# Kernel tuning notes

Hardware: AMD Instinct MI355X
Metric: run time of the kernel (lower is better)

## Reference

```python
import jax, jax.numpy as jnp
import numpy as np

B, S, D_IN, D_H, D_OUT = 8, 4096, 512, 1024, 512


def setup_inputs() -> dict:
    key = jax.random.key(0)
    ks = jax.random.split(key, 7)
    # scale weights by 1/sqrt(fan_in) so activations stay O(1) through the ReLU stack
    return {
        "query": jax.random.normal(ks[0], (B, S, D_IN), dtype=jnp.float32),
        "W0": jax.random.normal(ks[1], (B, D_H, D_IN), dtype=jnp.float32) * (D_IN ** -0.5),
        "b0": jax.random.normal(ks[2], (B, D_H), dtype=jnp.float32) * 0.02,
        "W1": jax.random.normal(ks[3], (B, D_H, D_H), dtype=jnp.float32) * (D_H ** -0.5),
        "b1": jax.random.normal(ks[4], (B, D_H), dtype=jnp.float32) * 0.02,
        "W2": jax.random.normal(ks[5], (B, D_OUT, D_H), dtype=jnp.float32) * (D_H ** -0.5),
        "b2": jax.random.normal(ks[6], (B, D_OUT), dtype=jnp.float32) * 0.02,
    }


def reference(query, W0, b0, W1, b1, W2, b2):
    # Original loops over (seq, batch) issuing F.linear per sample with per-batch
    # weights; this is exactly a batched GEMM over the batch axis.
    # F.linear(x, w, b) = x @ w.T + b, with w[b] of shape [out, in].
    h = jax.nn.relu(jnp.einsum('bsd,bhd->bsh', query, W0) + b0[:, None, :])  # [B,S,H]
    h = jax.nn.relu(jnp.einsum('bsh,bgh->bsg', h, W1) + b1[:, None, :])      # [B,S,H]
    out = jnp.einsum('bsg,bog->bso', h, W2) + b2[:, None, :]                 # [B,S,O]
    return out
```

## Files before the change

### kernel.cpp

```cpp
#include <hip/hip_runtime.h>


typedef _Float16 f16x8 __attribute__((ext_vector_type(8)));
typedef _Float16 f16x4 __attribute__((ext_vector_type(4)));
typedef float    f32x4 __attribute__((ext_vector_type(4)));

__device__ __forceinline__ void stage16(const void* g, void* l) {
    __builtin_amdgcn_global_load_lds(
        (const __attribute__((address_space(1))) unsigned int*)g,
        (__attribute__((address_space(3))) unsigned int*)l,
        16, 0, 0);
}

template <int CNT> __device__ __forceinline__ void vmwait() {
    if constexpr (CNT == 8)      asm volatile("s_waitcnt vmcnt(8)");
    else if constexpr (CNT == 4) asm volatile("s_waitcnt vmcnt(4)");
    else                         asm volatile("s_waitcnt vmcnt(0)");
}
__device__ __forceinline__ void barrier_() {
    __builtin_amdgcn_sched_barrier(0);
    __builtin_amdgcn_s_barrier();
}

__device__ __forceinline__ void cast_seg(const float* __restrict__ s,
                                         _Float16* __restrict__ d, int n4) {
    const int stride = gridDim.x * 256;
    for (int i = blockIdx.x * 256 + threadIdx.x; i < n4; i += stride) {
        float4 f = reinterpret_cast<const float4*>(s)[i];
        f16x4 o;
        o[0] = (_Float16)f.x; o[1] = (_Float16)f.y;
        o[2] = (_Float16)f.z; o[3] = (_Float16)f.w;
        reinterpret_cast<f16x4*>(d)[i] = o;
    }
}

__global__ __launch_bounds__(256) void cast_all(
    const float* s0, _Float16* d0, int n0,
    const float* s1, _Float16* d1, int n1,
    const float* s2, _Float16* d2, int n2,
    const float* s3, _Float16* d3, int n3) {
    cast_seg(s0, d0, n0);
    cast_seg(s1, d1, n1);
    cast_seg(s2, d2, n2);
    cast_seg(s3, d3, n3);
}

template <bool RELU, bool OUT_F16>
__global__ __launch_bounds__(512, 2) void gemm_olap(
    const _Float16* __restrict__ A, const _Float16* __restrict__ W,
    const float* __restrict__ bias, void* __restrict__ Outv,
    int M, int N, int K) {
    constexpr int BM = 256, BN = 256, BK = 32;
    constexpr int DEPTH = 4;
    __shared__ __align__(16) _Float16 As[DEPTH][BM * BK];
    __shared__ __align__(16) _Float16 Bs[DEPTH][BN * BK];

    const int tid  = threadIdx.x;
    const int lane = tid & 63;
    const int rowl = lane & 15;
    const int qswz = (((lane >> 4) ^ ((rowl >> 1) & 3)) * 8);
    const int w    = tid >> 6;
    const int wm   = (w >> 2) * 128;
    const int wn   = (w & 3) * 64;

    const int nwg = gridDim.x;
    const int cpx = nwg >> 3;
    const int sw  = (blockIdx.x & 7) * cpx + (blockIdx.x >> 3);
    const int MB  = M >> 8;
    const int NB  = N >> 8;
    const int bm  = sw % MB;
    const int rr  = sw / MB;
    const int bn  = rr % NB;
    const int b   = rr / NB;

    const int c0 = tid, c1 = tid + 512;
    const int ar0 = c0 >> 2, ar1 = c1 >> 2;
    const int ak0 = (((c0 & 3) ^ ((ar0 >> 1) & 3)) * 8);
    const int ak1 = (((c1 & 3) ^ ((ar1 >> 1) & 3)) * 8);

    const char* Ab = (const char*)(A + (size_t)b * M * K + (size_t)(bm * BM) * K);
    const char* Wb = (const char*)(W + (size_t)b * N * K + (size_t)(bn * BN) * K);
    size_t aoff0 = ((size_t)ar0 * K + ak0) * 2;
    size_t aoff1 = ((size_t)ar1 * K + ak1) * 2;
    size_t woff0 = ((size_t)ar0 * K + ak0) * 2;
    size_t woff1 = ((size_t)ar1 * K + ak1) * 2;
    constexpr size_t KSTEP = (size_t)BK * 2;

    f32x4 acc[8][4];
#pragma unroll
    for (int mi = 0; mi < 8; ++mi)
#pragma unroll
        for (int ni = 0; ni < 4; ++ni)
            acc[mi][ni] = (f32x4){0.f, 0.f, 0.f, 0.f};

    const int nk = K / BK;

#pragma unroll
    for (int p = 0; p < DEPTH - 1; ++p) {
        stage16(Ab + aoff0, &As[p][8 * (size_t)c0]);
        stage16(Ab + aoff1, &As[p][8 * (size_t)c1]);
        stage16(Wb + woff0, &Bs[p][8 * (size_t)c0]);
        stage16(Wb + woff1, &Bs[p][8 * (size_t)c1]);
        aoff0 += KSTEP; aoff1 += KSTEP; woff0 += KSTEP; woff1 += KSTEP;
    }
    vmwait<8>();
    barrier_();

    f16x8 afA[8], bfA[4], afB[8], bfB[4];

#define READS(AF, BF, SS)                                                     \
    BF[0] = *(const f16x8*)(&Bs[SS][(wn +  0 + rowl) * BK + qswz]);           \
    BF[1] = *(const f16x8*)(&Bs[SS][(wn + 16 + rowl) * BK + qswz]);           \
    BF[2] = *(const f16x8*)(&Bs[SS][(wn + 32 + rowl) * BK + qswz]);           \
    BF[3] = *(const f16x8*)(&Bs[SS][(wn + 48 + rowl) * BK + qswz]);           \
    _Pragma("unroll")                                                         \
    for (int mi = 0; mi < 8; ++mi)                                            \
        AF[mi] = *(const f16x8*)(&As[SS][(wm + mi * 16 + rowl) * BK + qswz]);

#define STAGE(SS)                                                             \
    stage16(Ab + aoff0, &As[SS][8 * (size_t)c0]);                             \
    stage16(Ab + aoff1, &As[SS][8 * (size_t)c1]);                             \
    stage16(Wb + woff0, &Bs[SS][8 * (size_t)c0]);                             \
    stage16(Wb + woff1, &Bs[SS][8 * (size_t)c1]);                             \
    aoff0 += KSTEP; aoff1 += KSTEP; woff0 += KSTEP; woff1 += KSTEP;

#define MFMA32(AF, BF)                                                        \
    __builtin_amdgcn_s_setprio(1);                                            \
    _Pragma("unroll")                                                         \
    for (int mi = 0; mi < 8; ++mi) {                                          \
        acc[mi][0] = __builtin_amdgcn_mfma_f32_16x16x32_f16(AF[mi], BF[0], acc[mi][0], 0, 0, 0); \
        acc[mi][1] = __builtin_amdgcn_mfma_f32_16x16x32_f16(AF[mi], BF[1], acc[mi][1], 0, 0, 0); \
        acc[mi][2] = __builtin_amdgcn_mfma_f32_16x16x32_f16(AF[mi], BF[2], acc[mi][2], 0, 0, 0); \
        acc[mi][3] = __builtin_amdgcn_mfma_f32_16x16x32_f16(AF[mi], BF[3], acc[mi][3], 0, 0, 0); \
    }                                                                         \
    __builtin_amdgcn_s_setprio(0);

    READS(afA, bfA, 0);

    for (int i = 0; i < nk / 2; ++i) {
        const int t0 = 2 * i, t1 = t0 + 1;

        if (t0 + 2 < nk) vmwait<4>(); else vmwait<0>();
        barrier_();
        if (t0 + 3 < nk) { STAGE((t0 + 3) & 3); }
        READS(afB, bfB, t1 & 3);
        MFMA32(afA, bfA);

        if (t1 + 2 < nk) vmwait<4>(); else vmwait<0>();
        barrier_();
        if (t1 + 3 < nk) { STAGE((t1 + 3) & 3); }
        if (t1 + 1 < nk) { READS(afA, bfA, (t1 + 1) & 3); }
        MFMA32(afB, bfB);
    }
#undef READS
#undef STAGE
#undef MFMA32

    const int q = lane >> 4;
    float bcol[4];
    {
        const float* bp = bias + (size_t)b * N + bn * BN + wn;
#pragma unroll
        for (int ni = 0; ni < 4; ++ni) bcol[ni] = bp[ni * 16 + rowl];
    }
#pragma unroll
    for (int mi = 0; mi < 8; ++mi) {
        const int row0 = bm * BM + wm + mi * 16 + q * 4;
#pragma unroll
        for (int r = 0; r < 4; ++r) {
            const size_t ro = (size_t)b * M * N + (size_t)(row0 + r) * N + bn * BN + wn;
#pragma unroll
            for (int ni = 0; ni < 4; ++ni) {
                float v = acc[mi][ni][r] + bcol[ni];
                if (RELU) v = fmaxf(v, 0.f);
                if (OUT_F16)
                    ((_Float16*)Outv)[ro + ni * 16 + rowl] = (_Float16)v;
                else
                    ((float*)Outv)[ro + ni * 16 + rowl] = v;
            }
        }
    }
}

__device__ __forceinline__ uint4 load8f32(const char* p) {
    const float4* fp = reinterpret_cast<const float4*>(p);
    float4 f0 = fp[0], f1 = fp[1];
    f16x8 o;
    o[0] = (_Float16)f0.x; o[1] = (_Float16)f0.y;
    o[2] = (_Float16)f0.z; o[3] = (_Float16)f0.w;
    o[4] = (_Float16)f1.x; o[5] = (_Float16)f1.y;
    o[6] = (_Float16)f1.z; o[7] = (_Float16)f1.w;
    return __builtin_bit_cast(uint4, o);
}

template <bool A_F16, bool W_F16, bool RELU, bool OUT_F16>
__global__ __launch_bounds__(256) void gemm_bias_act(
    const void* __restrict__ Av, const void* __restrict__ Wv,
    const float* __restrict__ bias, void* __restrict__ Outv,
    int M, int N, int K) {
    constexpr int BM = 128, BN = 128, BK = 32;
    __shared__ __align__(16) _Float16 As[BM * BK];
    __shared__ __align__(16) _Float16 Bs[BN * BK];

    const int tid  = threadIdx.x;
    const int lane = tid & 63;
    const int rowl = lane & 15;
    const int q8   = (lane >> 4) * 8;
    const int wm   = ((tid >> 6) >> 1) * 64;
    const int wn   = ((tid >> 6) & 1) * 64;
    const int bm = blockIdx.x, bn = blockIdx.y, b = blockIdx.z;

    const int c0 = tid, c1 = tid + 256;
    const int ar0 = c0 >> 2, ak0 = (c0 & 3) * 8;
    const int ar1 = c1 >> 2, ak1 = (c1 & 3) * 8;

    constexpr size_t esA = A_F16 ? 2 : 4;
    constexpr size_t esW = W_F16 ? 2 : 4;
    const char* Abase = (const char*)Av;
    const char* Wbase = (const char*)Wv;

    size_t aoff0 = ((size_t)b * M * K + (size_t)(bm * BM + ar0) * K + ak0) * esA;
    size_t aoff1 = ((size_t)b * M * K + (size_t)(bm * BM + ar1) * K + ak1) * esA;
    size_t woff0 = ((size_t)b * N * K + (size_t)(bn * BN + ar0) * K + ak0) * esW;
    size_t woff1 = ((size_t)b * N * K + (size_t)(bn * BN + ar1) * K + ak1) * esW;

    f32x4 acc[4][4];
#pragma unroll
    for (int mi = 0; mi < 4; ++mi)
#pragma unroll
        for (int ni = 0; ni < 4; ++ni)
            acc[mi][ni] = (f32x4){0.f, 0.f, 0.f, 0.f};

    const int nk = K / BK;
    for (int kk = 0; kk < nk; ++kk) {
        uint4 va0, va1, vw0, vw1;
        if (!A_F16) { va0 = load8f32(Abase + aoff0); va1 = load8f32(Abase + aoff1); }
        if (!W_F16) { vw0 = load8f32(Wbase + woff0); vw1 = load8f32(Wbase + woff1); }
        __syncthreads();
        if (A_F16) {
            stage16(Abase + aoff0, As + 8 * (size_t)c0);
            stage16(Abase + aoff1, As + 8 * (size_t)c1);
        } else {
            *(uint4*)(As + ar0 * BK + ak0) = va0;
            *(uint4*)(As + ar1 * BK + ak1) = va1;
        }
        if (W_F16) {
            stage16(Wbase + woff0, Bs + 8 * (size_t)c0);
            stage16(Wbase + woff1, Bs + 8 * (size_t)c1);
        } else {
            *(uint4*)(Bs + ar0 * BK + ak0) = vw0;
            *(uint4*)(Bs + ar1 * BK + ak1) = vw1;
        }
        aoff0 += BK * esA; aoff1 += BK * esA;
        woff0 += BK * esW; woff1 += BK * esW;
        __syncthreads();

        f16x8 af[4], bf[4];
#pragma unroll
        for (int i = 0; i < 4; ++i)
            af[i] = *(const f16x8*)(As + (wm + i * 16 + rowl) * BK + q8);
#pragma unroll
        for (int i = 0; i < 4; ++i)
            bf[i] = *(const f16x8*)(Bs + (wn + i * 16 + rowl) * BK + q8);
#pragma unroll
        for (int mi = 0; mi < 4; ++mi)
#pragma unroll
            for (int ni = 0; ni < 4; ++ni)
                acc[mi][ni] = __builtin_amdgcn_mfma_f32_16x16x32_f16(
                    af[mi], bf[ni], acc[mi][ni], 0, 0, 0);
    }

    const int q = lane >> 4;
    float bcol[4];
    {
        const float* bp = bias + (size_t)b * N + bn * BN + wn;
#pragma unroll
        for (int ni = 0; ni < 4; ++ni) bcol[ni] = bp[ni * 16 + rowl];
    }
#pragma unroll
    for (int mi = 0; mi < 4; ++mi) {
        const int row0 = bm * BM + wm + mi * 16 + q * 4;
#pragma unroll
        for (int r = 0; r < 4; ++r) {
            const size_t ro = (size_t)b * M * N + (size_t)(row0 + r) * N + bn * BN + wn;
#pragma unroll
            for (int ni = 0; ni < 4; ++ni) {
                float v = acc[mi][ni][r] + bcol[ni];
                if (RELU) v = fmaxf(v, 0.f);
                if (OUT_F16)
                    ((_Float16*)Outv)[ro + ni * 16 + rowl] = (_Float16)v;
                else
                    ((float*)Outv)[ro + ni * 16 + rowl] = v;
            }
        }
    }
}

extern "C" void kernel_launch(void* const* d_in, const int* in_sizes, int n_in,
                              void* d_out, int out_size, void* d_ws, size_t ws_size,
                              hipStream_t stream) {
    const int B = 8, S = 4096, DI = 512, DH = 1024, DO = 512;
    const float* query = (const float*)d_in[0];
    const float* W0    = (const float*)d_in[1];
    const float* b0    = (const float*)d_in[2];
    const float* W1    = (const float*)d_in[3];
    const float* b1    = (const float*)d_in[4];
    const float* W2    = (const float*)d_in[5];
    const float* b2    = (const float*)d_in[6];

    char* ws = (char*)d_ws;
    const size_t nH  = (size_t)B * S * DH;
    const size_t nQ  = (size_t)B * S * DI;
    const size_t nW0 = (size_t)B * DH * DI;
    const size_t nW1 = (size_t)B * DH * DH;
    const size_t nW2 = (size_t)B * DO * DH;

    _Float16* h0 = (_Float16*)ws;
    _Float16* h1 = (_Float16*)(ws + nH * 2);
    const size_t off_casts = nH * 4;
    const size_t full_need = off_casts + (nQ + nW0 + nW1 + nW2) * 2;

    if (ws_size >= full_need) {
        _Float16* qf  = (_Float16*)(ws + off_casts);
        _Float16* w0f = qf + nQ;
        _Float16* w1f = w0f + nW0;
        _Float16* w2f = w1f + nW1;
        cast_all<<<dim3(2048), dim3(256), 0, stream>>>(
            query, qf, (int)(nQ / 4), W0, w0f, (int)(nW0 / 4),
            W1, w1f, (int)(nW1 / 4), W2, w2f, (int)(nW2 / 4));
        const dim3 blk(512);
        const dim3 g0(dim3((S / 256) * (DH / 256) * B));
        const dim3 g2(dim3((S / 256) * (DO / 256) * B));
        gemm_olap<true,  true ><<<g0, blk, 0, stream>>>(qf, w0f, b0, h0, S, DH, DI);
        gemm_olap<true,  true ><<<g0, blk, 0, stream>>>(h0, w1f, b1, h1, S, DH, DH);
        gemm_olap<false, false><<<g2, blk, 0, stream>>>(h1, w2f, b2, d_out, S, DO, DH);
    } else {
        const dim3 blk(256);
        const dim3 g0(S / 128, DH / 128, B);
        const dim3 g2(S / 128, DO / 128, B);
        gemm_bias_act<false, false, true,  true ><<<g0, blk, 0, stream>>>(query, W0, b0, h0, S, DH, DI);
        gemm_bias_act<true,  false, true,  true ><<<g0, blk, 0, stream>>>(h0, W1, b1, h1, S, DH, DH);
        gemm_bias_act<true,  false, false, false><<<g2, blk, 0, stream>>>(h1, W2, b2, d_out, S, DO, DH);
    }
}
```

Before: 346.6 us.

## Use 16-wave workgroups with 32x32x16 MFMA and single-step pipelined main loop

Rewrites the main GEMM kernel to run 1024 threads (16 waves) per 256x256 tile. Each wave now owns a 64x64 sub-tile computed with 32x32x16 MFMA instructions instead of a 128x64 sub-tile built from 16x16x32 ones. The K loop is restructured to one stage per iteration, with each thread issuing one A and one B async LDS load and the waitcnt adjusted to match. The aim is more latency hiding through more waves and fewer LDS reads per FLOP from the larger MFMA shape. The costs are more barrier participants, less register-level reuse per wave, and a different LDS swizzle read pattern.

```diff
diff --git a/kernel.cpp b/kernel.cpp
--- a/kernel.cpp
+++ b/kernel.cpp
@@ -4,6 +4,7 @@
 typedef _Float16 f16x8 __attribute__((ext_vector_type(8)));
 typedef _Float16 f16x4 __attribute__((ext_vector_type(4)));
 typedef float    f32x4 __attribute__((ext_vector_type(4)));
+typedef float    f32x16 __attribute__((ext_vector_type(16)));
 
 __device__ __forceinline__ void stage16(const void* g, void* l) {
     __builtin_amdgcn_global_load_lds(
@@ -13,8 +14,8 @@
 }
 
 template <int CNT> __device__ __forceinline__ void vmwait() {
-    if constexpr (CNT == 8)      asm volatile("s_waitcnt vmcnt(8)");
-    else if constexpr (CNT == 4) asm volatile("s_waitcnt vmcnt(4)");
+    if constexpr (CNT == 4)      asm volatile("s_waitcnt vmcnt(4)");
+    else if constexpr (CNT == 2) asm volatile("s_waitcnt vmcnt(2)");
     else                         asm volatile("s_waitcnt vmcnt(0)");
 }
 __device__ __forceinline__ void barrier_() {
@@ -46,7 +47,7 @@
 }
 
 template <bool RELU, bool OUT_F16>
-__global__ __launch_bounds__(512, 2) void gemm_olap(
+__global__ __launch_bounds__(1024, 4) void gemm_w16(
     const _Float16* __restrict__ A, const _Float16* __restrict__ W,
     const float* __restrict__ bias, void* __restrict__ Outv,
     int M, int N, int K) {
@@ -57,11 +58,19 @@
 
     const int tid  = threadIdx.x;
     const int lane = tid & 63;
-    const int rowl = lane & 15;
-    const int qswz = (((lane >> 4) ^ ((rowl >> 1) & 3)) * 8);
+    const int l31  = lane & 31;
+    const int kg   = lane >> 5;
+    const int sx   = (l31 >> 1) & 3;
     const int w    = tid >> 6;
-    const int wm   = (w >> 2) * 128;
+    const int wm   = (w >> 2) * 64;
     const int wn   = (w & 3) * 64;
+
+    const int kch0 = ((0 + kg) ^ sx) * 8;
+    const int kch1 = ((2 + kg) ^ sx) * 8;
+    const int aoffr0 = (wm +  0 + l31) * BK;
+    const int aoffr1 = (wm + 32 + l31) * BK;
+    const int boffr0 = (wn +  0 + l31) * BK;
+    const int boffr1 = (wn + 32 + l31) * BK;
 
     const int nwg = gridDim.x;
     const int cpx = nwg >> 3;
@@ -73,113 +82,89 @@
     const int bn  = rr % NB;
     const int b   = rr / NB;
 
-    const int c0 = tid, c1 = tid + 512;
-    const int ar0 = c0 >> 2, ar1 = c1 >> 2;
-    const int ak0 = (((c0 & 3) ^ ((ar0 >> 1) & 3)) * 8);
-    const int ak1 = (((c1 & 3) ^ ((ar1 >> 1) & 3)) * 8);
+    const int srow = tid >> 2;
+    const int skcg = (tid & 3) ^ ((srow >> 1) & 3);
 
     const char* Ab = (const char*)(A + (size_t)b * M * K + (size_t)(bm * BM) * K);
     const char* Wb = (const char*)(W + (size_t)b * N * K + (size_t)(bn * BN) * K);
-    size_t aoff0 = ((size_t)ar0 * K + ak0) * 2;
-    size_t aoff1 = ((size_t)ar1 * K + ak1) * 2;
-    size_t woff0 = ((size_t)ar0 * K + ak0) * 2;
-    size_t woff1 = ((size_t)ar1 * K + ak1) * 2;
+    size_t goff = ((size_t)srow * K + skcg * 8) * 2;
     constexpr size_t KSTEP = (size_t)BK * 2;
 
-    f32x4 acc[8][4];
-#pragma unroll
-    for (int mi = 0; mi < 8; ++mi)
-#pragma unroll
-        for (int ni = 0; ni < 4; ++ni)
-            acc[mi][ni] = (f32x4){0.f, 0.f, 0.f, 0.f};
+    f32x16 acc[2][2];
+#pragma unroll
+    for (int mi = 0; mi < 2; ++mi)
+#pragma unroll
+        for (int ni = 0; ni < 2; ++ni)
+            acc[mi][ni] = (f32x16){0.f, 0.f, 0.f, 0.f, 0.f, 0.f, 0.f, 0.f,
+                                   0.f, 0.f, 0.f, 0.f, 0.f, 0.f, 0.f, 0.f};
 
     const int nk = K / BK;
 
 #pragma unroll
     for (int p = 0; p < DEPTH - 1; ++p) {
-        stage16(Ab + aoff0, &As[p][8 * (size_t)c0]);
-        stage16(Ab + aoff1, &As[p][8 * (size_t)c1]);
-        stage16(Wb + woff0, &Bs[p][8 * (size_t)c0]);
-        stage16(Wb + woff1, &Bs[p][8 * (size_t)c1]);
-        aoff0 += KSTEP; aoff1 += KSTEP; woff0 += KSTEP; woff1 += KSTEP;
-    }
-    vmwait<8>();
+        stage16(Ab + goff, &As[p][8 * (size_t)tid]);
+        stage16(Wb + goff, &Bs[p][8 * (size_t)tid]);
+        goff += KSTEP;
+    }
+    vmwait<4>();
     barrier_();
 
-    f16x8 afA[8], bfA[4], afB[8], bfB[4];
-
-#define READS(AF, BF, SS)                                                     \
-    BF[0] = *(const f16x8*)(&Bs[SS][(wn +  0 + rowl) * BK + qswz]);           \
-    BF[1] = *(const f16x8*)(&Bs[SS][(wn + 16 + rowl) * BK + qswz]);           \
-    BF[2] = *(const f16x8*)(&Bs[SS][(wn + 32 + rowl) * BK + qswz]);           \
-    BF[3] = *(const f16x8*)(&Bs[SS][(wn + 48 + rowl) * BK + qswz]);           \
-    _Pragma("unroll")                                                         \
-    for (int mi = 0; mi < 8; ++mi)                                            \
-        AF[mi] = *(const f16x8*)(&As[SS][(wm + mi * 16 + rowl) * BK + qswz]);
-
-#define STAGE(SS)                                                             \
-    stage16(Ab + aoff0, &As[SS][8 * (size_t)c0]);                             \
-    stage16(Ab + aoff1, &As[SS][8 * (size_t)c1]);                             \
-    stage16(Wb + woff0, &Bs[SS][8 * (size_t)c0]);                             \
-    stage16(Wb + woff1, &Bs[SS][8 * (size_t)c1]);                             \
-    aoff0 += KSTEP; aoff1 += KSTEP; woff0 += KSTEP; woff1 += KSTEP;
-
-#define MFMA32(AF, BF)                                                        \
-    __builtin_amdgcn_s_setprio(1);                                            \
-    _Pragma("unroll")                                                         \
-    for (int mi = 0; mi < 8; ++mi) {                                          \
-        acc[mi][0] = __builtin_amdgcn_mfma_f32_16x16x32_f16(AF[mi], BF[0], acc[mi][0], 0, 0, 0); \
-        acc[mi][1] = __builtin_amdgcn_mfma_f32_16x16x32_f16(AF[mi], BF[1], acc[mi][1], 0, 0, 0); \
-        acc[mi][2] = __builtin_amdgcn_mfma_f32_16x16x32_f16(AF[mi], BF[2], acc[mi][2], 0, 0, 0); \
-        acc[mi][3] = __builtin_amdgcn_mfma_f32_16x16x32_f16(AF[mi], BF[3], acc[mi][3], 0, 0, 0); \
-    }                                                                         \
-    __builtin_amdgcn_s_setprio(0);
-
-    READS(afA, bfA, 0);
-
-    for (int i = 0; i < nk / 2; ++i) {
-        const int t0 = 2 * i, t1 = t0 + 1;
-
-        if (t0 + 2 < nk) vmwait<4>(); else vmwait<0>();
+    for (int t = 0; t < nk; ++t) {
+        const int slot = t & 3;
+
+        f16x8 a00 = *(const f16x8*)(&As[slot][aoffr0 + kch0]);
+        f16x8 a10 = *(const f16x8*)(&As[slot][aoffr1 + kch0]);
+        f16x8 a01 = *(const f16x8*)(&As[slot][aoffr0 + kch1]);
+        f16x8 a11 = *(const f16x8*)(&As[slot][aoffr1 + kch1]);
+        f16x8 b00 = *(const f16x8*)(&Bs[slot][boffr0 + kch0]);
+        f16x8 b10 = *(const f16x8*)(&Bs[slot][boffr1 + kch0]);
+        f16x8 b01 = *(const f16x8*)(&Bs[slot][boffr0 + kch1]);
+        f16x8 b11 = *(const f16x8*)(&Bs[slot][boffr1 + kch1]);
+
+        if (t + 3 < nk) {
+            const int ns = (t + 3) & 3;
+            stage16(Ab + goff, &As[ns][8 * (size_t)tid]);
+            stage16(Wb + goff, &Bs[ns][8 * (size_t)tid]);
+            goff += KSTEP;
+        }
         barrier_();
-        if (t0 + 3 < nk) { STAGE((t0 + 3) & 3); }
-        READS(afB, bfB, t1 & 3);
-        MFMA32(afA, bfA);
-
-        if (t1 + 2 < nk) vmwait<4>(); else vmwait<0>();
-        barrier_();
-        if (t1 + 3 < nk) { STAGE((t1 + 3) & 3); }
-        if (t1 + 1 < nk) { READS(afA, bfA, (t1 + 1) & 3); }
-        MFMA32(afB, bfB);
-    }
-#undef READS
-#undef STAGE
-#undef MFMA32
-
-    const int q = lane >> 4;
-    float bcol[4];
-    {
-        const float* bp = bias + (size_t)b * N + bn * BN + wn;
-#pragma unroll
-        for (int ni = 0; ni < 4; ++ni) bcol[ni] = bp[ni * 16 + rowl];
-    }
-#pragma unroll
-    for (int mi = 0; mi < 8; ++mi) {
-        const int row0 = bm * BM + wm + mi * 16 + q * 4;
-#pragma unroll
-        for (int r = 0; r < 4; ++r) {
-            const size_t ro = (size_t)b * M * N + (size_t)(row0 + r) * N + bn * BN + wn;
-#pragma unroll
-            for (int ni = 0; ni < 4; ++ni) {
-                float v = acc[mi][ni][r] + bcol[ni];
+
+        __builtin_amdgcn_s_setprio(1);
+        acc[0][0] = __builtin_amdgcn_mfma_f32_32x32x16_f16(a00, b00, acc[0][0], 0, 0, 0);
+        acc[0][1] = __builtin_amdgcn_mfma_f32_32x32x16_f16(a00, b10, acc[0][1], 0, 0, 0);
+        acc[1][0] = __builtin_amdgcn_mfma_f32_32x32x16_f16(a10, b00, acc[1][0], 0, 0, 0);
+        acc[1][1] = __builtin_amdgcn_mfma_f32_32x32x16_f16(a10, b10, acc[1][1], 0, 0, 0);
+        acc[0][0] = __builtin_amdgcn_mfma_f32_32x32x16_f16(a01, b01, acc[0][0], 0, 0, 0);
+        acc[0][1] = __builtin_amdgcn_mfma_f32_32x32x16_f16(a01, b11, acc[0][1], 0, 0, 0);
+        acc[1][0] = __builtin_amdgcn_mfma_f32_32x32x16_f16(a11, b01, acc[1][0], 0, 0, 0);
+        acc[1][1] = __builtin_amdgcn_mfma_f32_32x32x16_f16(a11, b11, acc[1][1], 0, 0, 0);
+        __builtin_amdgcn_s_setprio(0);
+
+        if (t + 3 < nk)      vmwait<4>();
+        else if (t + 2 < nk) vmwait<2>();
+        else if (t + 1 < nk) vmwait<0>();
+        if (t + 1 < nk) barrier_();
+    }
+
+#pragma unroll
+    for (int mi = 0; mi < 2; ++mi)
+#pragma unroll
+        for (int ni = 0; ni < 2; ++ni) {
+            const float bc = bias[(size_t)b * N + bn * BN + wn + ni * 32 + l31];
+            const size_t col = (size_t)bn * BN + wn + ni * 32 + l31;
+            const int row0 = bm * BM + wm + mi * 32 + 4 * kg;
+#pragma unroll
+            for (int r = 0; r < 16; ++r) {
+                const int rowr = row0 + (r & 3) + 8 * (r >> 2);
+                const size_t ro = (size_t)b * M * N + (size_t)rowr * N + col;
+                float v = acc[mi][ni][r] + bc;
                 if (RELU) v = fmaxf(v, 0.f);
                 if (OUT_F16)
-                    ((_Float16*)Outv)[ro + ni * 16 + rowl] = (_Float16)v;
+                    ((_Float16*)Outv)[ro] = (_Float16)v;
                 else
-                    ((float*)Outv)[ro + ni * 16 + rowl] = v;
+                    ((float*)Outv)[ro] = v;
             }
         }
-    }
 }
 
 __device__ __forceinline__ uint4 load8f32(const char* p) {
@@ -328,12 +313,12 @@
         cast_all<<<dim3(2048), dim3(256), 0, stream>>>(
             query, qf, (int)(nQ / 4), W0, w0f, (int)(nW0 / 4),
             W1, w1f, (int)(nW1 / 4), W2, w2f, (int)(nW2 / 4));
-        const dim3 blk(512);
+        const dim3 blk(1024);
         const dim3 g0(dim3((S / 256) * (DH / 256) * B));
         const dim3 g2(dim3((S / 256) * (DO / 256) * B));
-        gemm_olap<true,  true ><<<g0, blk, 0, stream>>>(qf, w0f, b0, h0, S, DH, DI);
-        gemm_olap<true,  true ><<<g0, blk, 0, stream>>>(h0, w1f, b1, h1, S, DH, DH);
-        gemm_olap<false, false><<<g2, blk, 0, stream>>>(h1, w2f, b2, d_out, S, DO, DH);
+        gemm_w16<true,  true ><<<g0, blk, 0, stream>>>(qf, w0f, b0, h0, S, DH, DI);
+        gemm_w16<true,  true ><<<g0, blk, 0, stream>>>(h0, w1f, b1, h1, S, DH, DH);
+        gemm_w16<false, false><<<g2, blk, 0, stream>>>(h1, w2f, b2, d_out, S, DO, DH);
     } else {
         const dim3 blk(256);
         const dim3 g0(S / 128, DH / 128, B);
```

Measured after the change: 348.9 us. Within noise of the previous version (+0.7%).

## Restructure GEMM mainloop into BK=64 double-buffer with quadrant-interleaved loads and MFMAs

Applied to the files above, without the earlier changes.

Replaces the 4-deep BK=32 LDS ring with a 2-buffer BK=64 scheme. Each k-step is split into four quadrant phases, with the next tile's global-to-LDS loads spread between the MFMA blocks and a new 8-slot XOR swizzle for the 64-wide rows. The aim is to overlap global loads with matrix math more finely and to halve the number of k iterations. It adds many barriers per iteration, and the shallower prefetch depth may expose memory latency.

```diff
diff --git a/kernel.cpp b/kernel.cpp
--- a/kernel.cpp
+++ b/kernel.cpp
@@ -13,8 +13,8 @@
 }
 
 template <int CNT> __device__ __forceinline__ void vmwait() {
-    if constexpr (CNT == 8)      asm volatile("s_waitcnt vmcnt(8)");
-    else if constexpr (CNT == 4) asm volatile("s_waitcnt vmcnt(4)");
+    if constexpr (CNT == 4)      asm volatile("s_waitcnt vmcnt(4)");
+    else if constexpr (CNT == 2) asm volatile("s_waitcnt vmcnt(2)");
     else                         asm volatile("s_waitcnt vmcnt(0)");
 }
 __device__ __forceinline__ void barrier_() {
@@ -46,22 +46,23 @@
 }
 
 template <bool RELU, bool OUT_F16>
-__global__ __launch_bounds__(512, 2) void gemm_olap(
+__global__ __launch_bounds__(512, 2) void gemm_q4(
     const _Float16* __restrict__ A, const _Float16* __restrict__ W,
     const float* __restrict__ bias, void* __restrict__ Outv,
     int M, int N, int K) {
-    constexpr int BM = 256, BN = 256, BK = 32;
-    constexpr int DEPTH = 4;
-    __shared__ __align__(16) _Float16 As[DEPTH][BM * BK];
-    __shared__ __align__(16) _Float16 Bs[DEPTH][BN * BK];
+    constexpr int BM = 256, BN = 256, BK = 64;
+    __shared__ __align__(16) _Float16 As[2][BM * BK];
+    __shared__ __align__(16) _Float16 Bs[2][BN * BK];
 
     const int tid  = threadIdx.x;
     const int lane = tid & 63;
     const int rowl = lane & 15;
-    const int qswz = (((lane >> 4) ^ ((rowl >> 1) & 3)) * 8);
+    const int q    = lane >> 4;
+    const int slotx = rowl & 7;
     const int w    = tid >> 6;
     const int wm   = (w >> 2) * 128;
     const int wn   = (w & 3) * 64;
+    const int amId = w >> 2;
 
     const int nwg = gridDim.x;
     const int cpx = nwg >> 3;
@@ -73,18 +74,24 @@
     const int bn  = rr % NB;
     const int b   = rr / NB;
 
-    const int c0 = tid, c1 = tid + 512;
-    const int ar0 = c0 >> 2, ar1 = c1 >> 2;
-    const int ak0 = (((c0 & 3) ^ ((ar0 >> 1) & 3)) * 8);
-    const int ak1 = (((c1 & 3) ^ ((ar1 >> 1) & 3)) * 8);
+    const int gtidA = (w & 3) * 64 + lane;
+    const int gA    = (gtidA & 7) ^ ((gtidA >> 3) & 7);
+    const int rowA0 = amId * 128 + (gtidA >> 3);
+    const int gtidB = (w >> 2) * 64 + lane;
+    const int gB    = (gtidB & 7) ^ ((gtidB >> 3) & 7);
+    const int rowB0 = wn + (gtidB >> 3);
 
     const char* Ab = (const char*)(A + (size_t)b * M * K + (size_t)(bm * BM) * K);
     const char* Wb = (const char*)(W + (size_t)b * N * K + (size_t)(bn * BN) * K);
-    size_t aoff0 = ((size_t)ar0 * K + ak0) * 2;
-    size_t aoff1 = ((size_t)ar1 * K + ak1) * 2;
-    size_t woff0 = ((size_t)ar0 * K + ak0) * 2;
-    size_t woff1 = ((size_t)ar1 * K + ak1) * 2;
-    constexpr size_t KSTEP = (size_t)BK * 2;
+    size_t aG = ((size_t)rowA0 * K + gA * 8) * 2;
+    size_t bG = ((size_t)rowB0 * K + gB * 8) * 2;
+    const size_t AKROW = (size_t)32 * K * 2;
+    const size_t BKROW = (size_t)16 * K * 2;
+    const int ldsA0 = (amId * 1024 + (w & 3) * 64 + lane) * 8;
+    const int ldsB0 = (wn * 8 + (w >> 2) * 64 + lane) * 8;
+
+#define STA(BUF, KI) stage16(Ab + aG + (KI) * AKROW, &As[BUF][ldsA0 + (KI) * 2048])
+#define STB(BUF, KI) stage16(Wb + bG + (KI) * BKROW, &Bs[BUF][ldsB0 + (KI) * 1024])
 
     f32x4 acc[8][4];
 #pragma unroll
@@ -95,68 +102,80 @@
 
     const int nk = K / BK;
 
-#pragma unroll
-    for (int p = 0; p < DEPTH - 1; ++p) {
-        stage16(Ab + aoff0, &As[p][8 * (size_t)c0]);
-        stage16(Ab + aoff1, &As[p][8 * (size_t)c1]);
-        stage16(Wb + woff0, &Bs[p][8 * (size_t)c0]);
-        stage16(Wb + woff1, &Bs[p][8 * (size_t)c1]);
-        aoff0 += KSTEP; aoff1 += KSTEP; woff0 += KSTEP; woff1 += KSTEP;
-    }
-    vmwait<8>();
+    STB(0, 0); STB(0, 1); STB(0, 2); STB(0, 3);
+    STA(0, 0); STA(0, 1); STA(0, 2); STA(0, 3);
+    aG += 128; bG += 128;
+    vmwait<2>();
     barrier_();
 
-    f16x8 afA[8], bfA[4], afB[8], bfB[4];
-
-#define READS(AF, BF, SS)                                                     \
-    BF[0] = *(const f16x8*)(&Bs[SS][(wn +  0 + rowl) * BK + qswz]);           \
-    BF[1] = *(const f16x8*)(&Bs[SS][(wn + 16 + rowl) * BK + qswz]);           \
-    BF[2] = *(const f16x8*)(&Bs[SS][(wn + 32 + rowl) * BK + qswz]);           \
-    BF[3] = *(const f16x8*)(&Bs[SS][(wn + 48 + rowl) * BK + qswz]);           \
+#define RDA(MI0, SS)                                                          \
     _Pragma("unroll")                                                         \
-    for (int mi = 0; mi < 8; ++mi)                                            \
-        AF[mi] = *(const f16x8*)(&As[SS][(wm + mi * 16 + rowl) * BK + qswz]);
-
-#define STAGE(SS)                                                             \
-    stage16(Ab + aoff0, &As[SS][8 * (size_t)c0]);                             \
-    stage16(Ab + aoff1, &As[SS][8 * (size_t)c1]);                             \
-    stage16(Wb + woff0, &Bs[SS][8 * (size_t)c0]);                             \
-    stage16(Wb + woff1, &Bs[SS][8 * (size_t)c1]);                             \
-    aoff0 += KSTEP; aoff1 += KSTEP; woff0 += KSTEP; woff1 += KSTEP;
-
-#define MFMA32(AF, BF)                                                        \
+    for (int m2 = 0; m2 < 4; ++m2) {                                          \
+        const int ro = (wm + ((MI0) + m2) * 16 + rowl) * 64;                  \
+        af[m2][0] = *(const f16x8*)(&As[SS][ro + (((0 * 4 + q) ^ slotx) * 8)]);\
+        af[m2][1] = *(const f16x8*)(&As[SS][ro + (((1 * 4 + q) ^ slotx) * 8)]);\
+    }
+#define RDB(NI0, SS)                                                          \
+    _Pragma("unroll")                                                         \
+    for (int n2 = 0; n2 < 2; ++n2) {                                          \
+        const int ro = (wn + ((NI0) + n2) * 16 + rowl) * 64;                  \
+        bf[(NI0) + n2][0] = *(const f16x8*)(&Bs[SS][ro + (((0 * 4 + q) ^ slotx) * 8)]);\
+        bf[(NI0) + n2][1] = *(const f16x8*)(&Bs[SS][ro + (((1 * 4 + q) ^ slotx) * 8)]);\
+    }
+#define MF(MH, NH)                                                            \
     __builtin_amdgcn_s_setprio(1);                                            \
     _Pragma("unroll")                                                         \
-    for (int mi = 0; mi < 8; ++mi) {                                          \
-        acc[mi][0] = __builtin_amdgcn_mfma_f32_16x16x32_f16(AF[mi], BF[0], acc[mi][0], 0, 0, 0); \
-        acc[mi][1] = __builtin_amdgcn_mfma_f32_16x16x32_f16(AF[mi], BF[1], acc[mi][1], 0, 0, 0); \
-        acc[mi][2] = __builtin_amdgcn_mfma_f32_16x16x32_f16(AF[mi], BF[2], acc[mi][2], 0, 0, 0); \
-        acc[mi][3] = __builtin_amdgcn_mfma_f32_16x16x32_f16(AF[mi], BF[3], acc[mi][3], 0, 0, 0); \
-    }                                                                         \
+    for (int m2 = 0; m2 < 4; ++m2)                                            \
+        _Pragma("unroll")                                                     \
+        for (int n2 = 0; n2 < 2; ++n2) {                                      \
+            acc[(MH)*4+m2][(NH)*2+n2] = __builtin_amdgcn_mfma_f32_16x16x32_f16(\
+                af[m2][0], bf[(NH)*2+n2][0], acc[(MH)*4+m2][(NH)*2+n2], 0,0,0);\
+            acc[(MH)*4+m2][(NH)*2+n2] = __builtin_amdgcn_mfma_f32_16x16x32_f16(\
+                af[m2][1], bf[(NH)*2+n2][1], acc[(MH)*4+m2][(NH)*2+n2], 0,0,0);\
+        }                                                                     \
     __builtin_amdgcn_s_setprio(0);
 
-    READS(afA, bfA, 0);
-
-    for (int i = 0; i < nk / 2; ++i) {
-        const int t0 = 2 * i, t1 = t0 + 1;
-
-        if (t0 + 2 < nk) vmwait<4>(); else vmwait<0>();
-        barrier_();
-        if (t0 + 3 < nk) { STAGE((t0 + 3) & 3); }
-        READS(afB, bfB, t1 & 3);
-        MFMA32(afA, bfA);
-
-        if (t1 + 2 < nk) vmwait<4>(); else vmwait<0>();
-        barrier_();
-        if (t1 + 3 < nk) { STAGE((t1 + 3) & 3); }
-        if (t1 + 1 < nk) { READS(afA, bfA, (t1 + 1) & 3); }
-        MFMA32(afB, bfB);
-    }
-#undef READS
-#undef STAGE
-#undef MFMA32
-
-    const int q = lane >> 4;
+    f16x8 af[4][2], bf[4][2];
+
+    for (int t = 0; t < nk; ++t) {
+        const int cb  = t & 1;
+        const int sb  = cb ^ 1;
+        const bool stg = (t + 1 < nk);
+
+        RDB(0, cb);
+        RDA(0, cb);
+        if (stg) { STB(sb, 0); STB(sb, 1); }
+        barrier_();
+        MF(0, 0);
+        barrier_();
+
+        RDB(2, cb);
+        if (stg) { STB(sb, 2); STB(sb, 3); }
+        barrier_();
+        MF(0, 1);
+        if (stg) vmwait<4>(); else vmwait<0>();
+        barrier_();
+
+        RDA(4, cb);
+        if (stg) { STA(sb, 0); STA(sb, 1); }
+        barrier_();
+        MF(1, 0);
+        barrier_();
+
+        if (stg) { STA(sb, 2); STA(sb, 3); }
+        barrier_();
+        MF(1, 1);
+        if (stg) { vmwait<2>(); }
+        barrier_();
+        aG += 128; bG += 128;
+    }
+#undef RDA
+#undef RDB
+#undef MF
+#undef STA
+#undef STB
+
+    const int qq = lane >> 4;
     float bcol[4];
     {
         const float* bp = bias + (size_t)b * N + bn * BN + wn;
@@ -165,7 +184,7 @@
     }
 #pragma unroll
     for (int mi = 0; mi < 8; ++mi) {
-        const int row0 = bm * BM + wm + mi * 16 + q * 4;
+        const int row0 = bm * BM + wm + mi * 16 + qq * 4;
 #pragma unroll
         for (int r = 0; r < 4; ++r) {
             const size_t ro = (size_t)b * M * N + (size_t)(row0 + r) * N + bn * BN + wn;
@@ -331,9 +350,9 @@
         const dim3 blk(512);
         const dim3 g0(dim3((S / 256) * (DH / 256) * B));
         const dim3 g2(dim3((S / 256) * (DO / 256) * B));
-        gemm_olap<true,  true ><<<g0, blk, 0, stream>>>(qf, w0f, b0, h0, S, DH, DI);
-        gemm_olap<true,  true ><<<g0, blk, 0, stream>>>(h0, w1f, b1, h1, S, DH, DH);
-        gemm_olap<false, false><<<g2, blk, 0, stream>>>(h1, w2f, b2, d_out, S, DO, DH);
+        gemm_q4<true,  true ><<<g0, blk, 0, stream>>>(qf, w0f, b0, h0, S, DH, DI);
+        gemm_q4<true,  true ><<<g0, blk, 0, stream>>>(h0, w1f, b1, h1, S, DH, DH);
+        gemm_q4<false, false><<<g2, blk, 0, stream>>>(h1, w2f, b2, d_out, S, DO, DH);
     } else {
         const dim3 blk(256);
         const dim3 g0(S / 128, DH / 128, B);
```

New measurement: 319.1 us. 7.9% less time.
